# Performance work log

Measured on AMD Instinct MI355X. Metric: run time of the kernel, lower is better.

The kernel has to match this reference:

```python
import jax, jax.numpy as jnp
import numpy as np

N = 20000      # nodes
E = 320000     # edges per metapath graph
M = 3          # metapaths
IN = 256       # input feat dim
HID = 64       # num_hidden per head
NH = 4         # nhead (layer 1)
OUT = 256      # out_dim
NHO = 1        # nhead_out (layer 2)
SA_H = 128     # semantic attention hidden
NEG_SLOPE = 0.2


def gat_conv(h, W, attn_l, attn_r, src, dst, apply_relu):
    # h: [N, F_in]; W: [F_in, H*D]; attn_l/attn_r: [H, D]
    H, D = attn_l.shape
    feat = (h @ W).reshape(N, H, D)                      # [N, H, D]
    el = jnp.sum(feat * attn_l, axis=-1)                 # [N, H]
    er = jnp.sum(feat * attn_r, axis=-1)                 # [N, H]
    e = jax.nn.leaky_relu(el[src] + er[dst], NEG_SLOPE)  # [E, H]
    # edge softmax grouped by destination node
    emax = jax.ops.segment_max(e, dst, num_segments=N)   # [N, H] (-inf for empty)
    emax = jnp.where(jnp.isfinite(emax), emax, 0.0)
    ee = jnp.exp(e - emax[dst])                          # [E, H]
    denom = jax.ops.segment_sum(ee, dst, num_segments=N) # [N, H]
    alpha = ee / (denom[dst] + 1e-9)                     # [E, H]
    msg = alpha[:, :, None] * feat[src]                  # [E, H, D]
    out = jax.ops.segment_sum(msg, dst, num_segments=N)  # [N, H, D]
    out = out.reshape(N, H * D)                          # concat heads
    return jax.nn.relu(out) if apply_relu else out


def semantic_attention(z, W1, b1, v):
    # z: [N, M, F]
    w = jnp.tanh(z @ W1 + b1) @ v          # [N, M, 1]
    w = w.mean(axis=0)                     # [M, 1]
    beta = jax.nn.softmax(w, axis=0)       # [M, 1]
    out = jnp.sum(beta[None, :, :] * z, axis=1)  # [N, F]
    att_mp = beta.squeeze()                # [M]
    return out, att_mp


def setup_inputs() -> dict:
    key = jax.random.key(0)
    ks = jax.random.split(key, 16)
    s = 0.05
    return {
        "x": jax.random.normal(ks[0], (N, IN), dtype=jnp.float32),
        "edges": jax.random.randint(ks[1], (M, 2, E), 0, N, dtype=jnp.int64)
                 if jax.config.jax_enable_x64 else
                 jax.random.randint(ks[1], (M, 2, E), 0, N, dtype=jnp.int32),
        "W1": jax.random.normal(ks[2], (IN, NH * HID), dtype=jnp.float32) * s,
        "al1": jax.random.normal(ks[3], (NH, HID), dtype=jnp.float32) * s,
        "ar1": jax.random.normal(ks[4], (NH, HID), dtype=jnp.float32) * s,
        "saW1": jax.random.normal(ks[5], (NH * HID, SA_H), dtype=jnp.float32) * s,
        "sab1": jnp.zeros((SA_H,), dtype=jnp.float32),
        "sav1": jax.random.normal(ks[6], (SA_H, 1), dtype=jnp.float32) * s,
        "W2": jax.random.normal(ks[7], (NH * HID, NHO * OUT), dtype=jnp.float32) * s,
        "al2": jax.random.normal(ks[8], (NHO, OUT), dtype=jnp.float32) * s,
        "ar2": jax.random.normal(ks[9], (NHO, OUT), dtype=jnp.float32) * s,
        "saW2": jax.random.normal(ks[10], (NHO * OUT, SA_H), dtype=jnp.float32) * s,
        "sab2": jnp.zeros((SA_H,), dtype=jnp.float32),
        "sav2": jax.random.normal(ks[11], (SA_H, 1), dtype=jnp.float32) * s,
    }


def reference(x, edges, W1, al1, ar1, saW1, sab1, sav1,
              W2, al2, ar2, saW2, sab2, sav2):
    h = x
    # HAN layer 1: shared GATConv over each metapath graph, relu activation
    z = jnp.stack([gat_conv(h, W1, al1, ar1, edges[i, 0], edges[i, 1], True)
                   for i in range(M)], axis=1)          # [N, M, NH*HID]
    h, att_mp = semantic_attention(z, saW1, sab1, sav1)
    # HAN layer 2: last layer, no activation (encoding=False)
    z = jnp.stack([gat_conv(h, W2, al2, ar2, edges[i, 0], edges[i, 1], False)
                   for i in range(M)], axis=1)          # [N, M, NHO*OUT]
    h, att_mp = semantic_attention(z, saW2, sab2, sav2)
    return h, att_mp
```

## Files before the change

### kernel.cpp

```cpp
#include <hip/hip_runtime.h>
#include <hip/hip_bf16.h>
#include <math.h>

#define NN 20000
#define EE 320000
#define MM 3
#define FW 256
#define SAH 128
#define NB 79
#define RNG 2500

typedef __attribute__((ext_vector_type(8))) short bf16x8;
typedef __attribute__((ext_vector_type(4))) float f32x4;

static __device__ __forceinline__ float lrelu(float x){ return x > 0.f ? x : 0.2f*x; }

static __device__ __forceinline__ unsigned short f2bf(float f) {
    unsigned u = __float_as_uint(f);
    return (unsigned short)((u + 0x7FFFu + ((u >> 16) & 1u)) >> 16);
}
static __device__ __forceinline__ float bflo(unsigned u){ return __uint_as_float(u << 16); }
static __device__ __forceinline__ float bfhi(unsigned u){ return __uint_as_float(u & 0xffff0000u); }
static __device__ __forceinline__ unsigned pk2bf(float lo, float hi) {
    return ((unsigned)f2bf(lo)) | (((unsigned)f2bf(hi)) << 16);
}

#define XBLK 2500
__global__ __launch_bounds__(256) void prep_kernel(const float* __restrict__ x, unsigned short* __restrict__ xb,
                                                   const float* __restrict__ W1, unsigned short* __restrict__ W1t,
                                                   const float* __restrict__ saW1, unsigned short* __restrict__ saW1t,
                                                   const float* __restrict__ W2, unsigned short* __restrict__ W2t,
                                                   const float* __restrict__ saW2, unsigned short* __restrict__ saW2t) {
    int b = blockIdx.x, tid = threadIdx.x;
    if (b < XBLK) {
        int i = b*256 + tid;
        const float4* p = (const float4*)x + (size_t)i*2;
        float4 v0 = p[0], v1 = p[1];
        uint4 o;
        o.x = pk2bf(v0.x, v0.y); o.y = pk2bf(v0.z, v0.w);
        o.z = pk2bf(v1.x, v1.y); o.w = pk2bf(v1.z, v1.w);
        ((uint4*)xb)[i] = o;
        return;
    }
    int b2 = b - XBLK;
    if (b2 < 256)      { int n = b2;       W1t  [(size_t)n*256 + tid] = f2bf(W1  [(size_t)tid*256 + n]); }
    else if (b2 < 384) { int n = b2 - 256; saW1t[(size_t)n*256 + tid] = f2bf(saW1[(size_t)tid*SAH + n]); }
    else if (b2 < 640) { int n = b2 - 384; W2t  [(size_t)n*256 + tid] = f2bf(W2  [(size_t)tid*256 + n]); }
    else               { int n = b2 - 640; saW2t[(size_t)n*256 + tid] = f2bf(saW2[(size_t)tid*SAH + n]); }
}

__global__ __launch_bounds__(256) void hist_kernel(const int* __restrict__ edges, int* __restrict__ cnt) {
    int idx = blockIdx.x*256 + threadIdx.x;
    if (idx >= MM*EE/4) return;
    int m = idx / (EE/4), e4 = idx - m*(EE/4);
    int4 d = ((const int4*)(edges + (size_t)(m*2+1)*EE))[e4];
    atomicAdd(&cnt[m*NN + d.x], 1);
    atomicAdd(&cnt[m*NN + d.y], 1);
    atomicAdd(&cnt[m*NN + d.z], 1);
    atomicAdd(&cnt[m*NN + d.w], 1);
}

__global__ __launch_bounds__(256) void scanA_kernel(const int* __restrict__ cnt, int* __restrict__ rowptr, int* __restrict__ bsum) {
    int m = blockIdx.y;
    int i = blockIdx.x*256 + threadIdx.x;
    int v = (i < NN) ? cnt[m*NN + i] : 0;
    int lane = threadIdx.x & 63;
    int val = v;
    #pragma unroll
    for (int o = 1; o < 64; o <<= 1) { int t = __shfl_up(val, o); if (lane >= o) val += t; }
    __shared__ int ws[4];
    int w = threadIdx.x >> 6;
    if (lane == 63) ws[w] = val;
    __syncthreads();
    #pragma unroll
    for (int j = 0; j < 3; ++j) if (j < w) val += ws[j];
    if (i < NN) rowptr[m*(NN+1) + 1 + i] = val;
    if (threadIdx.x == 255) bsum[m*NB + blockIdx.x] = val;
}

__global__ __launch_bounds__(128) void scanB_kernel(const int* __restrict__ bsum, int* __restrict__ boff) {
    __shared__ int s[128];
    int t = threadIdx.x;
    for (int m = 0; m < MM; ++m) {
        int v = (t < NB) ? bsum[m*NB + t] : 0;
        s[t] = v; __syncthreads();
        for (int o = 1; o < 128; o <<= 1) {
            int x = (t >= o) ? s[t - o] : 0;
            __syncthreads();
            s[t] += x;
            __syncthreads();
        }
        if (t < NB) boff[m*NB + t] = s[t] - v;
        __syncthreads();
    }
}

__global__ __launch_bounds__(256) void scanC_kernel(const int* __restrict__ cnt, int* __restrict__ rowptr,
                                                    const int* __restrict__ boff, int* __restrict__ cursor) {
    int m = blockIdx.y;
    int i = blockIdx.x*256 + threadIdx.x;
    if (i >= NN) return;
    int incl = rowptr[m*(NN+1) + 1 + i] + boff[m*NB + blockIdx.x];
    rowptr[m*(NN+1) + 1 + i] = incl;
    cursor[m*NN + i] = incl - cnt[m*NN + i];
    if (i == 0 && blockIdx.x == 0) rowptr[m*(NN+1)] = 0;
}

__global__ __launch_bounds__(256) void scatter_kernel(const int* __restrict__ edges, int* __restrict__ cursor,
                                                      int* __restrict__ csr_src) {
    int m = blockIdx.y;
    int r = blockIdx.x & 7;
    int chunk = blockIdx.x >> 3;
    int e4 = chunk*256 + threadIdx.x;
    if (e4 >= EE/4) return;
    int lo = r * RNG, hi = lo + RNG;
    int4 s = ((const int4*)(edges + (size_t)(m*2  )*EE))[e4];
    int4 d = ((const int4*)(edges + (size_t)(m*2+1)*EE))[e4];
    if (d.x >= lo && d.x < hi) { int p = atomicAdd(&cursor[m*NN + d.x], 1); csr_src[(size_t)m*EE + p] = s.x; }
    if (d.y >= lo && d.y < hi) { int p = atomicAdd(&cursor[m*NN + d.y], 1); csr_src[(size_t)m*EE + p] = s.y; }
    if (d.z >= lo && d.z < hi) { int p = atomicAdd(&cursor[m*NN + d.z], 1); csr_src[(size_t)m*EE + p] = s.z; }
    if (d.w >= lo && d.w < hi) { int p = atomicAdd(&cursor[m*NN + d.w], 1); csr_src[(size_t)m*EE + p] = s.w; }
}

template<int H>
__global__ __launch_bounds__(256) void gemm_mfma_kernel(const unsigned short* __restrict__ A,
                                                        const unsigned short* __restrict__ Bt,
                                                        const float* __restrict__ attl, const float* __restrict__ attr,
                                                        unsigned short* __restrict__ C,
                                                        float* __restrict__ el, float* __restrict__ er) {
    int tid = threadIdx.x;
    int w = tid >> 6, lane = tid & 63;
    int rowgrp = w & 1, half = w >> 1;
    int r0 = blockIdx.x*32 + rowgrp*16;
    int colbase = half * 128;
    int lrow = lane & 15, lk = lane >> 4;

    bf16x8 a[8];
    const unsigned short* ap = A + (size_t)(r0 + lrow)*256 + lk*8;
    #pragma unroll
    for (int k = 0; k < 8; ++k) a[k] = *(const bf16x8*)(ap + k*32);

    float pelv[2][4] = {{0.f,0.f,0.f,0.f},{0.f,0.f,0.f,0.f}};
    float perv[2][4] = {{0.f,0.f,0.f,0.f},{0.f,0.f,0.f,0.f}};

    #pragma unroll
    for (int n = 0; n < 8; ++n) {
        int col0 = colbase + n*16;
        const unsigned short* bp = Bt + (size_t)(col0 + lrow)*256 + lk*8;
        f32x4 acc = {0.f, 0.f, 0.f, 0.f};
        #pragma unroll
        for (int k = 0; k < 8; ++k) {
            bf16x8 bfr = *(const bf16x8*)(bp + k*32);
            acc = __builtin_amdgcn_mfma_f32_16x16x32_bf16(a[k], bfr, acc, 0, 0, 0);
        }
        int col = col0 + lrow;
        float al = attl[col], ar = attr[col];
        int hl = (H == 4) ? (n >> 2) : 0;
        #pragma unroll
        for (int r = 0; r < 4; ++r) {
            float cv = acc[r];
            pelv[hl][r] += cv * al;
            perv[hl][r] += cv * ar;
            C[(size_t)(r0 + lk*4 + r)*256 + col] = f2bf(cv);
        }
    }

    int nhl = (H == 4) ? 2 : 1;
    #pragma unroll
    for (int hl = 0; hl < 2; ++hl) {
        if (hl >= nhl) break;
        #pragma unroll
        for (int r = 0; r < 4; ++r) {
            float pe = pelv[hl][r], pr = perv[hl][r];
            #pragma unroll
            for (int o = 1; o < 16; o <<= 1) { pe += __shfl_xor(pe, o); pr += __shfl_xor(pr, o); }
            pelv[hl][r] = pe; perv[hl][r] = pr;
        }
    }

    if (H == 4) {
        if (lrow == 0) {
            int row = r0 + lk*4;
            #pragma unroll
            for (int hl = 0; hl < 2; ++hl) {
                int head = half*2 + hl;
                #pragma unroll
                for (int r = 0; r < 4; ++r) {
                    el[(size_t)(row + r)*4 + head] = pelv[hl][r];
                    er[(size_t)(row + r)*4 + head] = perv[hl][r];
                }
            }
        }
    } else {
        __shared__ float elds[2][32], erds[2][32];
        if (lrow == 0) {
            int rib = rowgrp*16 + lk*4;
            #pragma unroll
            for (int r = 0; r < 4; ++r) {
                elds[half][rib + r] = pelv[0][r];
                erds[half][rib + r] = perv[0][r];
            }
        }
        __syncthreads();
        if (tid < 32) {
            el[blockIdx.x*32 + tid] = elds[0][tid] + elds[1][tid];
            er[blockIdx.x*32 + tid] = erds[0][tid] + erds[1][tid];
        }
    }
}

template<int H>
__global__ __launch_bounds__(256) void edge_ee_kernel(const int* __restrict__ csr_src,
                                                      const int* __restrict__ rowptr,
                                                      const float* __restrict__ el, const float* __restrict__ er,
                                                      float* __restrict__ ee) {
    int m = blockIdx.y;
    int tid = threadIdx.x;
    int lane = tid & 63, wv = tid >> 6;
    int n = blockIdx.x*4 + wv;
    int beg = rowptr[m*(NN+1) + n], end = rowptr[m*(NN+1) + n + 1];
    const int eb = m*EE;
    if (H == 4) {
        float4 r4 = *(const float4*)&er[n*4];
        for (int e = beg + lane; e < end; e += 64) {
            int src = csr_src[eb + e];
            float4 l = *(const float4*)&el[src*4];
            float4 s;
            s.x = expf(lrelu(l.x + r4.x));
            s.y = expf(lrelu(l.y + r4.y));
            s.z = expf(lrelu(l.z + r4.z));
            s.w = expf(lrelu(l.w + r4.w));
            *(float4*)&ee[(size_t)(eb + e)*4] = s;
        }
    } else {
        float rn = er[n];
        for (int e = beg + lane; e < end; e += 64) {
            int src = csr_src[eb + e];
            ee[eb + e] = expf(lrelu(el[src] + rn));
        }
    }
}

template<int H, bool RELU>
__global__ __launch_bounds__(256) void agg_kernel(const unsigned short* __restrict__ feat,
                                                  const float* __restrict__ ee,
                                                  const int* __restrict__ rowptr,
                                                  const int* __restrict__ csr_src,
                                                  unsigned short* __restrict__ z) {
    int m = blockIdx.y;
    int tid = threadIdx.x;
    int lane = tid & 63, wv = tid >> 6;
    int n = blockIdx.x * 4 + wv;
    int eslot = lane >> 5, flane = lane & 31;
    int h = (H == 4) ? (flane >> 3) : 0;
    int beg = rowptr[m*(NN+1) + n], end = rowptr[m*(NN+1) + n + 1];
    const int eb = m*EE;

    float a[8] = {};
    float den = 0.f;
    int e0 = beg + eslot;

    int   sA = 0, sB = 0;
    float wA = 0.f, wB = 0.f;
    if (e0 < end)     { sA = csr_src[eb+e0  ]; wA = (H==4)? ee[(size_t)(eb+e0  )*4+h] : ee[eb+e0  ]; }
    if (e0 + 2 < end) { sB = csr_src[eb+e0+2]; wB = (H==4)? ee[(size_t)(eb+e0+2)*4+h] : ee[eb+e0+2]; }

    for (int e = e0; e < end; e += 2) {
        uint4 v = *(const uint4*)(feat + (size_t)sA*256 + flane*8);
        float w = wA;
        sA = sB; wA = wB;
        if (e + 4 < end) {
            sB = csr_src[eb+e+4];
            wB = (H==4)? ee[(size_t)(eb+e+4)*4+h] : ee[eb+e+4];
        }
        den += w;
        a[0] += w * bflo(v.x); a[1] += w * bfhi(v.x);
        a[2] += w * bflo(v.y); a[3] += w * bfhi(v.y);
        a[4] += w * bflo(v.z); a[5] += w * bfhi(v.z);
        a[6] += w * bflo(v.w); a[7] += w * bfhi(v.w);
    }

    #pragma unroll
    for (int j = 0; j < 8; ++j) a[j] += __shfl_xor(a[j], 32);
    den += __shfl_xor(den, 32);

    if (eslot == 0) {
        float inv = 1.f / (den + 1e-9f);
        #pragma unroll
        for (int j = 0; j < 8; ++j) {
            a[j] *= inv;
            if (RELU) a[j] = fmaxf(a[j], 0.f);
        }
        uint4 pk;
        pk.x = pk2bf(a[0], a[1]);
        pk.y = pk2bf(a[2], a[3]);
        pk.z = pk2bf(a[4], a[5]);
        pk.w = pk2bf(a[6], a[7]);
        *(uint4*)&z[((size_t)n*MM + m)*256 + flane*8] = pk;
    }
}

__global__ __launch_bounds__(256) void semw_mfma_kernel(const unsigned short* __restrict__ Z,
                                                        const unsigned short* __restrict__ Wt,
                                                        const float* __restrict__ bias, const float* __restrict__ v,
                                                        float* __restrict__ wsum) {
    int tid = threadIdx.x;
    int w = tid >> 6, lane = tid & 63;
    int r0 = blockIdx.x*64 + w*16;
    int lrow = lane & 15, lk = lane >> 4;

    int arow = r0 + lrow;
    if (arow >= NN*MM) arow = NN*MM - 1;
    bf16x8 a[8];
    const unsigned short* ap = Z + (size_t)arow*256 + lk*8;
    #pragma unroll
    for (int k = 0; k < 8; ++k) a[k] = *(const bf16x8*)(ap + k*32);

    float p[4] = {0.f, 0.f, 0.f, 0.f};
    #pragma unroll
    for (int n = 0; n < 8; ++n) {
        int col = n*16 + lrow;
        const unsigned short* bp = Wt + (size_t)col*256 + lk*8;
        f32x4 acc = {0.f, 0.f, 0.f, 0.f};
        #pragma unroll
        for (int k = 0; k < 8; ++k) {
            bf16x8 bfr = *(const bf16x8*)(bp + k*32);
            acc = __builtin_amdgcn_mfma_f32_16x16x32_bf16(a[k], bfr, acc, 0, 0, 0);
        }
        float bb = bias[col], vv = v[col];
        #pragma unroll
        for (int r = 0; r < 4; ++r)
            p[r] += tanhf(acc[r] + bb) * vv;
    }

    #pragma unroll
    for (int r = 0; r < 4; ++r) {
        #pragma unroll
        for (int o = 1; o < 16; o <<= 1) p[r] += __shfl_xor(p[r], o);
    }

    __shared__ float loc[3];
    if (tid < 3) loc[tid] = 0.f;
    __syncthreads();
    if (lrow == 0) {
        #pragma unroll
        for (int r = 0; r < 4; ++r) {
            int row = r0 + lk*4 + r;
            if (row < NN*MM) atomicAdd(&loc[row % MM], p[r]);
        }
    }
    __syncthreads();
    if (tid < 3) atomicAdd(&wsum[tid], loc[tid]);
}

__global__ void beta_kernel(const float* __restrict__ wsum, float* __restrict__ beta, float* att_out) {
    if (threadIdx.x == 0 && blockIdx.x == 0) {
        float w0 = wsum[0] / (float)NN, w1 = wsum[1] / (float)NN, w2 = wsum[2] / (float)NN;
        float mx = fmaxf(w0, fmaxf(w1, w2));
        float e0 = expf(w0 - mx), e1 = expf(w1 - mx), e2 = expf(w2 - mx);
        float s = e0 + e1 + e2;
        beta[0] = e0 / s; beta[1] = e1 / s; beta[2] = e2 / s;
        if (att_out) { att_out[0] = e0/s; att_out[1] = e1/s; att_out[2] = e2/s; }
    }
}

__global__ __launch_bounds__(128) void combine_bf16_kernel(const unsigned short* __restrict__ z, const float* __restrict__ beta,
                                                           unsigned short* __restrict__ outb) {
    int n = blockIdx.x, t = threadIdx.x;
    float b0 = beta[0], b1 = beta[1], b2 = beta[2];
    size_t base = (size_t)n*MM*256 + t*2;
    unsigned z0 = *(const unsigned*)&z[base];
    unsigned z1 = *(const unsigned*)&z[base + 256];
    unsigned z2 = *(const unsigned*)&z[base + 512];
    float ox = b0*bflo(z0) + b1*bflo(z1) + b2*bflo(z2);
    float oy = b0*bfhi(z0) + b1*bfhi(z1) + b2*bfhi(z2);
    *(unsigned*)&outb[(size_t)n*256 + t*2] = pk2bf(ox, oy);
}

__global__ __launch_bounds__(128) void combine_kernel(const unsigned short* __restrict__ z, const float* __restrict__ beta,
                                                      float* __restrict__ out) {
    int n = blockIdx.x, t = threadIdx.x;
    float b0 = beta[0], b1 = beta[1], b2 = beta[2];
    size_t base = (size_t)n*MM*256 + t*2;
    unsigned z0 = *(const unsigned*)&z[base];
    unsigned z1 = *(const unsigned*)&z[base + 256];
    unsigned z2 = *(const unsigned*)&z[base + 512];
    float2 o;
    o.x = b0*bflo(z0) + b1*bflo(z1) + b2*bflo(z2);
    o.y = b0*bfhi(z0) + b1*bfhi(z1) + b2*bfhi(z2);
    *(float2*)&out[(size_t)n*256 + t*2] = o;
}

extern "C" void kernel_launch(void* const* d_in, const int* in_sizes, int n_in,
                              void* d_out, int out_size, void* d_ws, size_t ws_size,
                              hipStream_t stream) {
    const float* x    = (const float*)d_in[0];
    const int*   edges= (const int*)  d_in[1];
    const float* W1   = (const float*)d_in[2];
    const float* al1  = (const float*)d_in[3];
    const float* ar1  = (const float*)d_in[4];
    const float* saW1 = (const float*)d_in[5];
    const float* sab1 = (const float*)d_in[6];
    const float* sav1 = (const float*)d_in[7];
    const float* W2   = (const float*)d_in[8];
    const float* al2  = (const float*)d_in[9];
    const float* ar2  = (const float*)d_in[10];
    const float* saW2 = (const float*)d_in[11];
    const float* sab2 = (const float*)d_in[12];
    const float* sav2 = (const float*)d_in[13];
    float* out = (float*)d_out;

    char* ws = (char*)d_ws;
    size_t off = 0;
    auto alloc = [&](size_t bytes) { void* p = ws + off; off += (bytes + 255) & ~(size_t)255; return p; };
    unsigned short* feat  = (unsigned short*)alloc((size_t)NN*256*2);
    unsigned short* z     = (unsigned short*)alloc((size_t)NN*MM*256*2);
    unsigned short* xb    = (unsigned short*)alloc((size_t)NN*256*2);
    unsigned short* W1t   = (unsigned short*)alloc(256*256*2);
    unsigned short* saW1t = (unsigned short*)alloc(SAH*256*2);
    unsigned short* W2t   = (unsigned short*)alloc(256*256*2);
    unsigned short* saW2t = (unsigned short*)alloc(SAH*256*2);
    float* ee     = (float*)alloc((size_t)MM*EE*4*4);
    float* el     = (float*)alloc(NN*4*4);
    float* er     = (float*)alloc(NN*4*4);
    float* wsum   = (float*)alloc(256);
    float* beta   = (float*)alloc(256);
    int*   cnt    = (int*)alloc(MM*NN*4);
    int*   cursor = (int*)alloc(MM*NN*4);
    int*   rowptr = (int*)alloc(MM*(NN+1)*4);
    int*   csr_s  = (int*)alloc((size_t)MM*EE*4);
    int*   bsum   = (int*)alloc(MM*NB*4);
    int*   boff   = (int*)alloc(MM*NB*4);
    unsigned short* hb = xb;

    int egrid4 = (MM*EE/4 + 255)/256;
    int chunks = (EE/4 + 255)/256;
    dim3 sg(NB, MM);

    prep_kernel<<<XBLK + 768, 256, 0, stream>>>(x, xb, W1, W1t, saW1, saW1t, W2, W2t, saW2, saW2t);

    hipMemsetAsync(cnt, 0, MM*NN*4, stream);
    hist_kernel<<<egrid4, 256, 0, stream>>>(edges, cnt);
    scanA_kernel<<<sg, 256, 0, stream>>>(cnt, rowptr, bsum);
    scanB_kernel<<<1, 128, 0, stream>>>(bsum, boff);
    scanC_kernel<<<sg, 256, 0, stream>>>(cnt, rowptr, boff, cursor);
    scatter_kernel<<<dim3(chunks*8, MM), 256, 0, stream>>>(edges, cursor, csr_s);

    gemm_mfma_kernel<4><<<NN/32, 256, 0, stream>>>(xb, W1t, al1, ar1, feat, el, er);
    edge_ee_kernel<4><<<dim3(NN/4, MM), 256, 0, stream>>>(csr_s, rowptr, el, er, ee);
    agg_kernel<4, true><<<dim3(NN/4, MM), 256, 0, stream>>>(feat, ee, rowptr, csr_s, z);
    hipMemsetAsync(wsum, 0, 16, stream);
    semw_mfma_kernel<<<(NN*MM + 63)/64, 256, 0, stream>>>(z, saW1t, sab1, sav1, wsum);
    beta_kernel<<<1, 64, 0, stream>>>(wsum, beta, nullptr);
    combine_bf16_kernel<<<NN, 128, 0, stream>>>(z, beta, hb);

    gemm_mfma_kernel<1><<<NN/32, 256, 0, stream>>>(hb, W2t, al2, ar2, feat, el, er);
    edge_ee_kernel<1><<<dim3(NN/4, MM), 256, 0, stream>>>(csr_s, rowptr, el, er, ee);
    agg_kernel<1, false><<<dim3(NN/4, MM), 256, 0, stream>>>(feat, ee, rowptr, csr_s, z);
    hipMemsetAsync(wsum, 0, 16, stream);
    semw_mfma_kernel<<<(NN*MM + 63)/64, 256, 0, stream>>>(z, saW2t, sab2, sav2, wsum);
    beta_kernel<<<1, 64, 0, stream>>>(wsum, beta, out + (size_t)NN*256);
    combine_kernel<<<NN, 128, 0, stream>>>(z, beta, out);
}
```

Measured before the change: 409.6 us.

## Fuse edge attention weight computation into aggregation kernel, unroll two edges

Removes the separate edge_ee kernel and the per-edge ee buffer. Each aggregation wave now computes exp(leaky_relu(el[src]+er[dst])) inline from a gathered el value. The loop is also restructured to process two edges per slot per iteration, with prefetch of the next source indices, to expose more memory-level parallelism. This avoids writing and re-reading the ee array and drops two launches. The cost is redundant exp work across the lanes sharing a head and an extra gather of el per edge.

```diff
diff --git a/kernel.cpp b/kernel.cpp
--- a/kernel.cpp
+++ b/kernel.cpp
@@ -209,41 +209,10 @@
     }
 }
 
-template<int H>
-__global__ __launch_bounds__(256) void edge_ee_kernel(const int* __restrict__ csr_src,
-                                                      const int* __restrict__ rowptr,
-                                                      const float* __restrict__ el, const float* __restrict__ er,
-                                                      float* __restrict__ ee) {
-    int m = blockIdx.y;
-    int tid = threadIdx.x;
-    int lane = tid & 63, wv = tid >> 6;
-    int n = blockIdx.x*4 + wv;
-    int beg = rowptr[m*(NN+1) + n], end = rowptr[m*(NN+1) + n + 1];
-    const int eb = m*EE;
-    if (H == 4) {
-        float4 r4 = *(const float4*)&er[n*4];
-        for (int e = beg + lane; e < end; e += 64) {
-            int src = csr_src[eb + e];
-            float4 l = *(const float4*)&el[src*4];
-            float4 s;
-            s.x = expf(lrelu(l.x + r4.x));
-            s.y = expf(lrelu(l.y + r4.y));
-            s.z = expf(lrelu(l.z + r4.z));
-            s.w = expf(lrelu(l.w + r4.w));
-            *(float4*)&ee[(size_t)(eb + e)*4] = s;
-        }
-    } else {
-        float rn = er[n];
-        for (int e = beg + lane; e < end; e += 64) {
-            int src = csr_src[eb + e];
-            ee[eb + e] = expf(lrelu(el[src] + rn));
-        }
-    }
-}
-
 template<int H, bool RELU>
 __global__ __launch_bounds__(256) void agg_kernel(const unsigned short* __restrict__ feat,
-                                                  const float* __restrict__ ee,
+                                                  const float* __restrict__ el,
+                                                  const float* __restrict__ er,
                                                   const int* __restrict__ rowptr,
                                                   const int* __restrict__ csr_src,
                                                   unsigned short* __restrict__ z) {
@@ -253,31 +222,38 @@
     int n = blockIdx.x * 4 + wv;
     int eslot = lane >> 5, flane = lane & 31;
     int h = (H == 4) ? (flane >> 3) : 0;
+    float ern = (H == 4) ? er[n*4 + h] : er[n];
     int beg = rowptr[m*(NN+1) + n], end = rowptr[m*(NN+1) + n + 1];
     const int eb = m*EE;
 
     float a[8] = {};
     float den = 0.f;
-    int e0 = beg + eslot;
-
+
+    int e = beg + eslot;
     int   sA = 0, sB = 0;
-    float wA = 0.f, wB = 0.f;
-    if (e0 < end)     { sA = csr_src[eb+e0  ]; wA = (H==4)? ee[(size_t)(eb+e0  )*4+h] : ee[eb+e0  ]; }
-    if (e0 + 2 < end) { sB = csr_src[eb+e0+2]; wB = (H==4)? ee[(size_t)(eb+e0+2)*4+h] : ee[eb+e0+2]; }
-
-    for (int e = e0; e < end; e += 2) {
-        uint4 v = *(const uint4*)(feat + (size_t)sA*256 + flane*8);
-        float w = wA;
-        sA = sB; wA = wB;
-        if (e + 4 < end) {
-            sB = csr_src[eb+e+4];
-            wB = (H==4)? ee[(size_t)(eb+e+4)*4+h] : ee[eb+e+4];
-        }
-        den += w;
-        a[0] += w * bflo(v.x); a[1] += w * bfhi(v.x);
-        a[2] += w * bflo(v.y); a[3] += w * bfhi(v.y);
-        a[4] += w * bflo(v.z); a[5] += w * bfhi(v.z);
-        a[6] += w * bflo(v.w); a[7] += w * bfhi(v.w);
+    float lA = 0.f, lB = 0.f;
+    if (e     < end) { sA = csr_src[eb+e  ];  lA = (H==4)? el[sA*4+h] : el[sA]; }
+    if (e + 2 < end) { sB = csr_src[eb+e+2];  lB = (H==4)? el[sB*4+h] : el[sB]; }
+
+    while (e < end) {
+        uint4 v0 = *(const uint4*)(feat + (size_t)sA*256 + flane*8);
+        bool h1 = (e + 2 < end);
+        uint4 v1 = make_uint4(0,0,0,0);
+        if (h1) v1 = *(const uint4*)(feat + (size_t)sB*256 + flane*8);
+        float w0 = expf(lrelu(lA + ern));
+        float w1 = h1 ? expf(lrelu(lB + ern)) : 0.f;
+        if (e + 4 < end) { sA = csr_src[eb+e+4]; lA = (H==4)? el[sA*4+h] : el[sA]; }
+        if (e + 6 < end) { sB = csr_src[eb+e+6]; lB = (H==4)? el[sB*4+h] : el[sB]; }
+        den += w0 + w1;
+        a[0] += w0*bflo(v0.x) + w1*bflo(v1.x);
+        a[1] += w0*bfhi(v0.x) + w1*bfhi(v1.x);
+        a[2] += w0*bflo(v0.y) + w1*bflo(v1.y);
+        a[3] += w0*bfhi(v0.y) + w1*bfhi(v1.y);
+        a[4] += w0*bflo(v0.z) + w1*bflo(v1.z);
+        a[5] += w0*bfhi(v0.z) + w1*bfhi(v1.z);
+        a[6] += w0*bflo(v0.w) + w1*bflo(v1.w);
+        a[7] += w0*bfhi(v0.w) + w1*bfhi(v1.w);
+        e += 4;
     }
 
     #pragma unroll
@@ -420,7 +396,6 @@
     unsigned short* saW1t = (unsigned short*)alloc(SAH*256*2);
     unsigned short* W2t   = (unsigned short*)alloc(256*256*2);
     unsigned short* saW2t = (unsigned short*)alloc(SAH*256*2);
-    float* ee     = (float*)alloc((size_t)MM*EE*4*4);
     float* el     = (float*)alloc(NN*4*4);
     float* er     = (float*)alloc(NN*4*4);
     float* wsum   = (float*)alloc(256);
@@ -447,16 +422,14 @@
     scatter_kernel<<<dim3(chunks*8, MM), 256, 0, stream>>>(edges, cursor, csr_s);
 
     gemm_mfma_kernel<4><<<NN/32, 256, 0, stream>>>(xb, W1t, al1, ar1, feat, el, er);
-    edge_ee_kernel<4><<<dim3(NN/4, MM), 256, 0, stream>>>(csr_s, rowptr, el, er, ee);
-    agg_kernel<4, true><<<dim3(NN/4, MM), 256, 0, stream>>>(feat, ee, rowptr, csr_s, z);
+    agg_kernel<4, true><<<dim3(NN/4, MM), 256, 0, stream>>>(feat, el, er, rowptr, csr_s, z);
     hipMemsetAsync(wsum, 0, 16, stream);
     semw_mfma_kernel<<<(NN*MM + 63)/64, 256, 0, stream>>>(z, saW1t, sab1, sav1, wsum);
     beta_kernel<<<1, 64, 0, stream>>>(wsum, beta, nullptr);
     combine_bf16_kernel<<<NN, 128, 0, stream>>>(z, beta, hb);
 
     gemm_mfma_kernel<1><<<NN/32, 256, 0, stream>>>(hb, W2t, al2, ar2, feat, el, er);
-    edge_ee_kernel<1><<<dim3(NN/4, MM), 256, 0, stream>>>(csr_s, rowptr, el, er, ee);
-    agg_kernel<1, false><<<dim3(NN/4, MM), 256, 0, stream>>>(feat, ee, rowptr, csr_s, z);
+    agg_kernel<1, false><<<dim3(NN/4, MM), 256, 0, stream>>>(feat, el, er, rowptr, csr_s, z);
     hipMemsetAsync(wsum, 0, 16, stream);
     semw_mfma_kernel<<<(NN*MM + 63)/64, 256, 0, stream>>>(z, saW2t, sab2, sav2, wsum);
     beta_kernel<<<1, 64, 0, stream>>>(wsum, beta, out + (size_t)NN*256);
```

Measured after the change: 410.7 us. Within noise of the previous version (+0.3%).
